# Performance work log

Hardware: AMD Instinct MI355X
Metric: run time of the kernel (lower is better)

Reference implementation:

```python
import jax, jax.numpy as jnp
import numpy as np

B, C, H, W = 4, 3, 512, 512
V, NF = 12000, 24000
UH, UW = 1024, 1024


def setup_inputs() -> dict:
    key = jax.random.key(0)
    ks = jax.random.split(key, 8)
    img = jax.random.normal(ks[0], (B, C, H, W), jnp.float32)
    mesh = jax.random.normal(ks[1], (B, V, 3), jnp.float32) * 0.3
    mesh = mesh.at[:, :, 2].add(3.0)  # keep depth positive so projection is well-defined
    face = jax.random.randint(ks[2], (NF, 3), 0, V, jnp.int32)
    focal = 800.0 + 200.0 * jax.random.uniform(ks[3], (B, 2), jnp.float32)
    princpt = jnp.tile(jnp.array([[W / 2.0, H / 2.0]], jnp.float32), (B, 1))
    R = jnp.tile(jnp.eye(3, dtype=jnp.float32)[None], (B, 1, 1))
    t = jnp.zeros((B, 3), jnp.float32)
    # pytorch3d packed convention: face id f of batch i is stored as f + NF*i, background = -1
    base = jax.random.randint(ks[4], (B, H, W), -1, NF, jnp.int32)
    offs = (NF * jnp.arange(B, dtype=jnp.int32))[:, None, None]
    pix_to_face_xy = jnp.where(base != -1, base + offs, -1)
    pix_to_face_uv = jax.random.randint(ks[5], (UH, UW), -1, NF, jnp.int32)
    bary = jax.random.uniform(ks[6], (UH, UW, 3), jnp.float32) + 1e-3
    bary_coords_uv = bary / bary.sum(-1, keepdims=True)
    return dict(img=img, mesh=mesh, face=face, focal=focal, princpt=princpt,
                R=R, t=t, pix_to_face_xy=pix_to_face_xy,
                pix_to_face_uv=pix_to_face_uv, bary_coords_uv=bary_coords_uv)


def _grid_sample(img, grid):
    # F.grid_sample: bilinear, align_corners=True, zero padding.
    # img [B,C,H,W], grid [B,Uh,Uw,2] in [-1,1] -> out [B,C,Uh,Uw]
    Bq, Cq, Hq, Wq = img.shape
    ix = (grid[..., 0] + 1.0) * 0.5 * (Wq - 1)
    iy = (grid[..., 1] + 1.0) * 0.5 * (Hq - 1)
    ix0 = jnp.floor(ix)
    iy0 = jnp.floor(iy)
    wx1 = ix - ix0
    wx0 = 1.0 - wx1
    wy1 = iy - iy0
    wy0 = 1.0 - wy1
    bidx = jnp.arange(Bq)[:, None, None]

    def tap(yf, xf, w):
        valid = (xf >= 0) & (xf <= Wq - 1) & (yf >= 0) & (yf <= Hq - 1)
        xi = jnp.clip(xf, 0, Wq - 1).astype(jnp.int32)
        yi = jnp.clip(yf, 0, Hq - 1).astype(jnp.int32)
        vals = img[bidx, :, yi, xi]  # [B,Uh,Uw,C]
        return vals * (w * valid)[..., None]

    out = (tap(iy0, ix0, wy0 * wx0) + tap(iy0, ix0 + 1.0, wy0 * wx1)
           + tap(iy0 + 1.0, ix0, wy1 * wx0) + tap(iy0 + 1.0, ix0 + 1.0, wy1 * wx1))
    return jnp.transpose(out, (0, 3, 1, 2))


def _forward(img, mesh, focal, princpt, R, t, bary_coords_uv,
             face, pix_to_face_xy, pix_to_face_uv):
    Bq, Cq, Hq, Wq = img.shape
    Fn = face.shape[0]
    Vn = mesh.shape[1]
    # camera transform + perspective projection
    mesh_cam = jnp.einsum('bij,bvj->bvi', R, mesh) + t[:, None, :]
    x = mesh_cam[..., 0] / mesh_cam[..., 2] * focal[:, None, 0] + princpt[:, None, 0]
    y = mesh_cam[..., 1] / mesh_cam[..., 2] * focal[:, None, 1] + princpt[:, None, 1]
    mesh_img = jnp.stack((x, y), 2)  # [B,V,2]
    # per-batch visible-face mask (packed ids: subtract Fn*i; torch's index -1 wraps
    # to face Fn-1 when scattering 1.0 -- replicate that exactly)
    local = jnp.where(pix_to_face_xy != -1,
                      pix_to_face_xy - Fn * jnp.arange(Bq, dtype=pix_to_face_xy.dtype)[:, None, None],
                      -1)
    local = jnp.where(local < 0, local + Fn, local)
    valid = jnp.zeros((Bq, Fn), jnp.float32).at[
        jnp.arange(Bq)[:, None], local.reshape(Bq, -1)].set(1.0)
    # invalidate invisible faces: vertex ids -> -1
    faces_b = jnp.where(valid[:, :, None] > 0, face[None].astype(jnp.int32), -1)  # [B,F,3]
    puv = jnp.where(pix_to_face_uv < 0, pix_to_face_uv + Fn, pix_to_face_uv)  # wrap like torch
    vidx = faces_b[:, puv, :]  # [B,UH,UW,3]
    invisible = (vidx[..., 0] == -1).astype(img.dtype)  # [B,UH,UW]
    vw = jnp.where(vidx < 0, vidx + Vn, vidx)  # -1 wraps to last vertex, like torch
    gathered = mesh_img[jnp.arange(Bq)[:, None, None, None], vw]  # [B,UH,UW,3,2]
    uvpos = jnp.einsum('bhwkc,hwk->bhwc', gathered, bary_coords_uv)  # barycentric blend
    grid = jnp.stack((uvpos[..., 0] / (Wq - 1) * 2.0 - 1.0,
                      uvpos[..., 1] / (Hq - 1) * 2.0 - 1.0), -1)
    uvmap = _grid_sample(img, grid)  # [B,C,UH,UW]
    uvmap = jnp.where((pix_to_face_uv == -1)[None, None], -1.0, uvmap)
    uvmap = uvmap * (1.0 - invisible)[:, None] - invisible[:, None]
    return uvmap


def reference(img, mesh, face, focal, princpt, R, t,
              pix_to_face_xy, pix_to_face_uv, bary_coords_uv):
    return _forward(img, mesh, focal, princpt, R, t, bary_coords_uv,
                    face, pix_to_face_xy, pix_to_face_uv)
```

## Files before the change

kernel.cpp:

```cpp
#include <hip/hip_runtime.h>

#define BQ 4
#define CQ 3
#define HQ 512
#define WQ 512
#define VN 12000
#define FN 24000
#define UHN 1024
#define UWN 1024
#define IMGPLANE (HQ * WQ)
#define VWORDS 768

typedef float fx4 __attribute__((ext_vector_type(4)));

#define MESHIMG_OFF 0u
#define VBITS_OFF   384000u
#define FD_OFF      396288u
#define IMGI_OFF    3468288u

__global__ void init_kernel(const float* __restrict__ mesh,
                            const float* __restrict__ focal,
                            const float* __restrict__ princpt,
                            const float* __restrict__ R,
                            const float* __restrict__ t,
                            float* __restrict__ mesh_img,
                            unsigned int* __restrict__ vbits) {
    int idx = blockIdx.x * blockDim.x + threadIdx.x;
    if (idx < BQ * VWORDS) vbits[idx] = 0u;
    if (idx >= BQ * VN) return;
    int b = idx / VN;
    const float* Rb = R + b * 9;
    const float* tb = t + b * 3;
    float mx = mesh[idx * 3 + 0];
    float my = mesh[idx * 3 + 1];
    float mz = mesh[idx * 3 + 2];
    float cx = Rb[0] * mx + Rb[1] * my + Rb[2] * mz + tb[0];
    float cy = Rb[3] * mx + Rb[4] * my + Rb[5] * mz + tb[1];
    float cz = Rb[6] * mx + Rb[7] * my + Rb[8] * mz + tb[2];
    float x = cx / cz * focal[b * 2 + 0] + princpt[b * 2 + 0];
    float y = cy / cz * focal[b * 2 + 1] + princpt[b * 2 + 1];
    mesh_img[idx * 2 + 0] = x;
    mesh_img[idx * 2 + 1] = y;
}

__global__ void interleave_kernel(const float* __restrict__ img,
                                  float4* __restrict__ img_i) {
    int i = blockIdx.x * blockDim.x + threadIdx.x;
    if (i >= (BQ * HQ * WQ) / 4) return;
    int g = i * 4;
    int b = g >> 18;
    int p = g & (IMGPLANE - 1);
    const float* ib = img + (size_t)b * CQ * IMGPLANE + p;
    float4 r0 = *(const float4*)(ib);
    float4 r1 = *(const float4*)(ib + IMGPLANE);
    float4 r2 = *(const float4*)(ib + 2 * IMGPLANE);
    img_i[g + 0] = make_float4(r0.x, r1.x, r2.x, 0.0f);
    img_i[g + 1] = make_float4(r0.y, r1.y, r2.y, 0.0f);
    img_i[g + 2] = make_float4(r0.z, r1.z, r2.z, 0.0f);
    img_i[g + 3] = make_float4(r0.w, r1.w, r2.w, 0.0f);
}

__global__ __launch_bounds__(256) void valid_kernel(const int4* __restrict__ ptf_xy4,
                                                    unsigned int* __restrict__ vbits) {
    __shared__ unsigned int lb[VWORDS];
    int tid = threadIdx.x;
    for (int i = tid; i < VWORDS; i += 256) lb[i] = 0u;
    __syncthreads();
    int b = blockIdx.x >> 6;
    int blkInB = blockIdx.x & 63;
    const int4* src = ptf_xy4 + ((size_t)b * IMGPLANE + blkInB * 4096) / 4;
#pragma unroll
    for (int k = 0; k < 4; ++k) {
        int4 p4 = src[tid + k * 256];
        int pv[4] = {p4.x, p4.y, p4.z, p4.w};
#pragma unroll
        for (int j = 0; j < 4; ++j) {
            int l = (pv[j] != -1) ? (pv[j] - FN * b) : -1;
            if (l < 0) l += FN;
            atomicOr(&lb[l >> 5], 1u << (l & 31));
        }
    }
    __syncthreads();
    for (int i = tid; i < VWORDS; i += 256) {
        unsigned int w = lb[i];
        if (w) atomicOr(&vbits[b * VWORDS + i], w);
    }
}

__global__ void fd_kernel(const int* __restrict__ face,
                          const float* __restrict__ mesh_img,
                          const unsigned int* __restrict__ vbits,
                          float4* __restrict__ fd) {
    int idx = blockIdx.x * blockDim.x + threadIdx.x;
    if (idx >= FN * BQ) return;
    int b = idx / FN;
    int f = idx - b * FN;
    int v0 = face[f * 3 + 0];
    int v1 = face[f * 3 + 1];
    int v2 = face[f * 3 + 2];
    const float* mi = mesh_img + (size_t)b * VN * 2;
    float4 a, c;
    a.x = mi[v0 * 2 + 0]; a.y = mi[v0 * 2 + 1];
    a.z = mi[v1 * 2 + 0]; a.w = mi[v1 * 2 + 1];
    c.x = mi[v2 * 2 + 0]; c.y = mi[v2 * 2 + 1];
    c.z = (float)((vbits[b * VWORDS + (f >> 5)] >> (f & 31)) & 1u);
    c.w = 0.0f;
    fd[(size_t)idx * 2 + 0] = a;
    fd[(size_t)idx * 2 + 1] = c;
}

__global__ __launch_bounds__(256) void uv_kernel(const float4* __restrict__ img_i,
                                                 const float4* __restrict__ fd,
                                                 const int* __restrict__ ptf_uv,
                                                 const float* __restrict__ bary,
                                                 float* __restrict__ out) {
    int blk = blockIdx.x;
    int r = blk & 7;
    int b = r >> 1;
    int pixBlk = ((blk >> 3) << 1) | (r & 1);
    int p0 = pixBlk * 1024 + (threadIdx.x << 2);

    const size_t PLANE = (size_t)UHN * UWN;

    int4 puv4 = *(const int4*)(ptf_uv + p0);
    float4 by0 = *(const float4*)(bary + (size_t)p0 * 3);
    float4 by1 = *(const float4*)(bary + (size_t)p0 * 3 + 4);
    float4 by2 = *(const float4*)(bary + (size_t)p0 * 3 + 8);

    int pin[4] = {puv4.x, puv4.y, puv4.z, puv4.w};
    float bw[12] = {by0.x, by0.y, by0.z, by0.w,
                    by1.x, by1.y, by1.z, by1.w,
                    by2.x, by2.y, by2.z, by2.w};

    const float4* fdb = fd + (size_t)b * FN * 2;
    float4 fa[4], fc[4];
    int pu[4];
#pragma unroll
    for (int k = 0; k < 4; ++k) {
        int p = pin[k];
        pu[k] = (p < 0) ? p + FN : p;
        fa[k] = fdb[pu[k] * 2 + 0];
        fc[k] = fdb[pu[k] * 2 + 1];
    }

    const float4* ibi = img_i + (size_t)b * IMGPLANE;
    float4 t00[4], t01[4], t10[4], t11[4];
    float g00[4], g01[4], g10[4], g11[4];
#pragma unroll
    for (int k = 0; k < 4; ++k) {
        float w0 = bw[3 * k + 0], w1 = bw[3 * k + 1], w2 = bw[3 * k + 2];
        float ux = w0 * fa[k].x + w1 * fa[k].z + w2 * fc[k].x;
        float uy = w0 * fa[k].y + w1 * fa[k].w + w2 * fc[k].y;

        float gx = ux / (float)(WQ - 1) * 2.0f - 1.0f;
        float gy = uy / (float)(HQ - 1) * 2.0f - 1.0f;
        float ix = (gx + 1.0f) * 0.5f * (float)(WQ - 1);
        float iy = (gy + 1.0f) * 0.5f * (float)(HQ - 1);

        float ix0 = floorf(ix), iy0 = floorf(iy);
        float wx1 = ix - ix0, wx0 = 1.0f - wx1;
        float wy1 = iy - iy0, wy0 = 1.0f - wy1;
        float ix1 = ix0 + 1.0f, iy1 = iy0 + 1.0f;

        bool x0ok = (ix0 >= 0.0f) && (ix0 <= (float)(WQ - 1));
        bool x1ok = (ix1 >= 0.0f) && (ix1 <= (float)(WQ - 1));
        bool y0ok = (iy0 >= 0.0f) && (iy0 <= (float)(HQ - 1));
        bool y1ok = (iy1 >= 0.0f) && (iy1 <= (float)(HQ - 1));

        g00[k] = (y0ok && x0ok) ? wy0 * wx0 : 0.0f;
        g01[k] = (y0ok && x1ok) ? wy0 * wx1 : 0.0f;
        g10[k] = (y1ok && x0ok) ? wy1 * wx0 : 0.0f;
        g11[k] = (y1ok && x1ok) ? wy1 * wx1 : 0.0f;

        int xi0 = (int)fminf(fmaxf(ix0, 0.0f), (float)(WQ - 1));
        int xi1 = (int)fminf(fmaxf(ix1, 0.0f), (float)(WQ - 1));
        int yi0 = (int)fminf(fmaxf(iy0, 0.0f), (float)(HQ - 1));
        int yi1 = (int)fminf(fmaxf(iy1, 0.0f), (float)(HQ - 1));

        t00[k] = ibi[yi0 * WQ + xi0];
        t01[k] = ibi[yi0 * WQ + xi1];
        t10[k] = ibi[yi1 * WQ + xi0];
        t11[k] = ibi[yi1 * WQ + xi1];
    }

    float o0[4], o1[4], o2[4];
#pragma unroll
    for (int k = 0; k < 4; ++k) {
        float acc0 = 0.f, acc1 = 0.f, acc2 = 0.f;
        acc0 += t00[k].x * g00[k]; acc1 += t00[k].y * g00[k]; acc2 += t00[k].z * g00[k];
        acc0 += t01[k].x * g01[k]; acc1 += t01[k].y * g01[k]; acc2 += t01[k].z * g01[k];
        acc0 += t10[k].x * g10[k]; acc1 += t10[k].y * g10[k]; acc2 += t10[k].z * g10[k];
        acc0 += t11[k].x * g11[k]; acc1 += t11[k].y * g11[k]; acc2 += t11[k].z * g11[k];
        bool ok = (pin[k] != -1) && (fc[k].z != 0.0f);
        o0[k] = ok ? acc0 : -1.0f;
        o1[k] = ok ? acc1 : -1.0f;
        o2[k] = ok ? acc2 : -1.0f;
    }

    float* ob = out + (size_t)b * CQ * PLANE + p0;
    fx4 s0 = {o0[0], o0[1], o0[2], o0[3]};
    fx4 s1 = {o1[0], o1[1], o1[2], o1[3]};
    fx4 s2 = {o2[0], o2[1], o2[2], o2[3]};
    __builtin_nontemporal_store(s0, (fx4*)(ob));
    __builtin_nontemporal_store(s1, (fx4*)(ob + PLANE));
    __builtin_nontemporal_store(s2, (fx4*)(ob + 2 * PLANE));
}

extern "C" void kernel_launch(void* const* d_in, const int* in_sizes, int n_in,
                              void* d_out, int out_size, void* d_ws, size_t ws_size,
                              hipStream_t stream) {
    const float* img     = (const float*)d_in[0];
    const float* mesh    = (const float*)d_in[1];
    const int*   face    = (const int*)d_in[2];
    const float* focal   = (const float*)d_in[3];
    const float* princpt = (const float*)d_in[4];
    const float* R       = (const float*)d_in[5];
    const float* t       = (const float*)d_in[6];
    const int*   ptf_xy  = (const int*)d_in[7];
    const int*   ptf_uv  = (const int*)d_in[8];
    const float* bary    = (const float*)d_in[9];
    float* out = (float*)d_out;

    unsigned char* ws = (unsigned char*)d_ws;
    float*         mesh_img = (float*)(ws + MESHIMG_OFF);
    unsigned int*  vbits    = (unsigned int*)(ws + VBITS_OFF);
    float4*        fd       = (float4*)(ws + FD_OFF);
    float4*        img_i    = (float4*)(ws + IMGI_OFF);

    init_kernel<<<(BQ * VN + 255) / 256, 256, 0, stream>>>(
        mesh, focal, princpt, R, t, mesh_img, vbits);

    interleave_kernel<<<(BQ * HQ * WQ / 4) / 256, 256, 0, stream>>>(img, img_i);

    valid_kernel<<<256, 256, 0, stream>>>((const int4*)ptf_xy, vbits);

    fd_kernel<<<(FN * BQ + 255) / 256, 256, 0, stream>>>(
        face, mesh_img, vbits, fd);

    uv_kernel<<<4096, 256, 0, stream>>>(img_i, fd, ptf_uv, bary, out);
}
```

Before: 188.5 us.

## Store interleaved image in fp16 and fuse prep kernels into one launch

The interleaved RGB image copy is now written as half precision (8 bytes per texel instead of 16), which halves the gather traffic in the bilinear-sample kernel and the write traffic of the interleave pass. The mesh projection and vbits clearing are merged into the interleave kernel, saving one launch. The uv kernel also switches its streaming input loads to nontemporal loads. Storing the image in fp16 loses precision in the sampled values and may exceed the accuracy tolerance.

```diff
diff --git a/kernel.cpp b/kernel.cpp
--- a/kernel.cpp
+++ b/kernel.cpp
@@ -11,53 +11,57 @@
 #define IMGPLANE (HQ * WQ)
 #define VWORDS 768
 
-typedef float fx4 __attribute__((ext_vector_type(4)));
+typedef float  fx4 __attribute__((ext_vector_type(4)));
+typedef int    ix4 __attribute__((ext_vector_type(4)));
+typedef _Float16 hx4 __attribute__((ext_vector_type(4)));
+typedef _Float16 hx8 __attribute__((ext_vector_type(8)));
 
 #define MESHIMG_OFF 0u
 #define VBITS_OFF   384000u
 #define FD_OFF      396288u
-#define IMGI_OFF    3468288u
-
-__global__ void init_kernel(const float* __restrict__ mesh,
-                            const float* __restrict__ focal,
-                            const float* __restrict__ princpt,
-                            const float* __restrict__ R,
-                            const float* __restrict__ t,
-                            float* __restrict__ mesh_img,
-                            unsigned int* __restrict__ vbits) {
-    int idx = blockIdx.x * blockDim.x + threadIdx.x;
-    if (idx < BQ * VWORDS) vbits[idx] = 0u;
-    if (idx >= BQ * VN) return;
-    int b = idx / VN;
-    const float* Rb = R + b * 9;
-    const float* tb = t + b * 3;
-    float mx = mesh[idx * 3 + 0];
-    float my = mesh[idx * 3 + 1];
-    float mz = mesh[idx * 3 + 2];
-    float cx = Rb[0] * mx + Rb[1] * my + Rb[2] * mz + tb[0];
-    float cy = Rb[3] * mx + Rb[4] * my + Rb[5] * mz + tb[1];
-    float cz = Rb[6] * mx + Rb[7] * my + Rb[8] * mz + tb[2];
-    float x = cx / cz * focal[b * 2 + 0] + princpt[b * 2 + 0];
-    float y = cy / cz * focal[b * 2 + 1] + princpt[b * 2 + 1];
-    mesh_img[idx * 2 + 0] = x;
-    mesh_img[idx * 2 + 1] = y;
-}
-
-__global__ void interleave_kernel(const float* __restrict__ img,
-                                  float4* __restrict__ img_i) {
-    int i = blockIdx.x * blockDim.x + threadIdx.x;
-    if (i >= (BQ * HQ * WQ) / 4) return;
+#define IMGH_OFF    3468288u
+
+__global__ __launch_bounds__(256) void prep_kernel(const float* __restrict__ img,
+                                                   const float* __restrict__ mesh,
+                                                   const float* __restrict__ focal,
+                                                   const float* __restrict__ princpt,
+                                                   const float* __restrict__ R,
+                                                   const float* __restrict__ t,
+                                                   float* __restrict__ mesh_img,
+                                                   unsigned int* __restrict__ vbits,
+                                                   _Float16* __restrict__ imgh) {
+    int i = blockIdx.x * 256 + threadIdx.x;
     int g = i * 4;
     int b = g >> 18;
     int p = g & (IMGPLANE - 1);
+
     const float* ib = img + (size_t)b * CQ * IMGPLANE + p;
     float4 r0 = *(const float4*)(ib);
     float4 r1 = *(const float4*)(ib + IMGPLANE);
     float4 r2 = *(const float4*)(ib + 2 * IMGPLANE);
-    img_i[g + 0] = make_float4(r0.x, r1.x, r2.x, 0.0f);
-    img_i[g + 1] = make_float4(r0.y, r1.y, r2.y, 0.0f);
-    img_i[g + 2] = make_float4(r0.z, r1.z, r2.z, 0.0f);
-    img_i[g + 3] = make_float4(r0.w, r1.w, r2.w, 0.0f);
+    hx8 s01 = {(_Float16)r0.x, (_Float16)r1.x, (_Float16)r2.x, (_Float16)0.f,
+               (_Float16)r0.y, (_Float16)r1.y, (_Float16)r2.y, (_Float16)0.f};
+    hx8 s23 = {(_Float16)r0.z, (_Float16)r1.z, (_Float16)r2.z, (_Float16)0.f,
+               (_Float16)r0.w, (_Float16)r1.w, (_Float16)r2.w, (_Float16)0.f};
+    *(hx8*)(imgh + (size_t)g * 4)       = s01;
+    *(hx8*)(imgh + (size_t)(g + 2) * 4) = s23;
+
+    if (i < BQ * VWORDS) vbits[i] = 0u;
+    if (i < BQ * VN) {
+        int bb = i / VN;
+        const float* Rb = R + bb * 9;
+        const float* tb = t + bb * 3;
+        float mx = mesh[i * 3 + 0];
+        float my = mesh[i * 3 + 1];
+        float mz = mesh[i * 3 + 2];
+        float cx = Rb[0] * mx + Rb[1] * my + Rb[2] * mz + tb[0];
+        float cy = Rb[3] * mx + Rb[4] * my + Rb[5] * mz + tb[1];
+        float cz = Rb[6] * mx + Rb[7] * my + Rb[8] * mz + tb[2];
+        float x = cx / cz * focal[bb * 2 + 0] + princpt[bb * 2 + 0];
+        float y = cy / cz * focal[bb * 2 + 1] + princpt[bb * 2 + 1];
+        mesh_img[i * 2 + 0] = x;
+        mesh_img[i * 2 + 1] = y;
+    }
 }
 
 __global__ __launch_bounds__(256) void valid_kernel(const int4* __restrict__ ptf_xy4,
@@ -109,7 +113,7 @@
     fd[(size_t)idx * 2 + 1] = c;
 }
 
-__global__ __launch_bounds__(256) void uv_kernel(const float4* __restrict__ img_i,
+__global__ __launch_bounds__(256) void uv_kernel(const _Float16* __restrict__ imgh,
                                                  const float4* __restrict__ fd,
                                                  const int* __restrict__ ptf_uv,
                                                  const float* __restrict__ bary,
@@ -122,15 +126,15 @@
 
     const size_t PLANE = (size_t)UHN * UWN;
 
-    int4 puv4 = *(const int4*)(ptf_uv + p0);
-    float4 by0 = *(const float4*)(bary + (size_t)p0 * 3);
-    float4 by1 = *(const float4*)(bary + (size_t)p0 * 3 + 4);
-    float4 by2 = *(const float4*)(bary + (size_t)p0 * 3 + 8);
-
-    int pin[4] = {puv4.x, puv4.y, puv4.z, puv4.w};
-    float bw[12] = {by0.x, by0.y, by0.z, by0.w,
-                    by1.x, by1.y, by1.z, by1.w,
-                    by2.x, by2.y, by2.z, by2.w};
+    ix4 puv4 = __builtin_nontemporal_load((const ix4*)(ptf_uv + p0));
+    fx4 by0 = __builtin_nontemporal_load((const fx4*)(bary + (size_t)p0 * 3));
+    fx4 by1 = __builtin_nontemporal_load((const fx4*)(bary + (size_t)p0 * 3 + 4));
+    fx4 by2 = __builtin_nontemporal_load((const fx4*)(bary + (size_t)p0 * 3 + 8));
+
+    int pin[4] = {puv4[0], puv4[1], puv4[2], puv4[3]};
+    float bw[12] = {by0[0], by0[1], by0[2], by0[3],
+                    by1[0], by1[1], by1[2], by1[3],
+                    by2[0], by2[1], by2[2], by2[3]};
 
     const float4* fdb = fd + (size_t)b * FN * 2;
     float4 fa[4], fc[4];
@@ -143,8 +147,8 @@
         fc[k] = fdb[pu[k] * 2 + 1];
     }
 
-    const float4* ibi = img_i + (size_t)b * IMGPLANE;
-    float4 t00[4], t01[4], t10[4], t11[4];
+    const _Float16* ihb = imgh + (size_t)b * IMGPLANE * 4;
+    hx4 t00[4], t01[4], t10[4], t11[4];
     float g00[4], g01[4], g10[4], g11[4];
 #pragma unroll
     for (int k = 0; k < 4; ++k) {
@@ -177,20 +181,20 @@
         int yi0 = (int)fminf(fmaxf(iy0, 0.0f), (float)(HQ - 1));
         int yi1 = (int)fminf(fmaxf(iy1, 0.0f), (float)(HQ - 1));
 
-        t00[k] = ibi[yi0 * WQ + xi0];
-        t01[k] = ibi[yi0 * WQ + xi1];
-        t10[k] = ibi[yi1 * WQ + xi0];
-        t11[k] = ibi[yi1 * WQ + xi1];
+        t00[k] = *(const hx4*)(ihb + (size_t)(yi0 * WQ + xi0) * 4);
+        t01[k] = *(const hx4*)(ihb + (size_t)(yi0 * WQ + xi1) * 4);
+        t10[k] = *(const hx4*)(ihb + (size_t)(yi1 * WQ + xi0) * 4);
+        t11[k] = *(const hx4*)(ihb + (size_t)(yi1 * WQ + xi1) * 4);
     }
 
     float o0[4], o1[4], o2[4];
 #pragma unroll
     for (int k = 0; k < 4; ++k) {
         float acc0 = 0.f, acc1 = 0.f, acc2 = 0.f;
-        acc0 += t00[k].x * g00[k]; acc1 += t00[k].y * g00[k]; acc2 += t00[k].z * g00[k];
-        acc0 += t01[k].x * g01[k]; acc1 += t01[k].y * g01[k]; acc2 += t01[k].z * g01[k];
-        acc0 += t10[k].x * g10[k]; acc1 += t10[k].y * g10[k]; acc2 += t10[k].z * g10[k];
-        acc0 += t11[k].x * g11[k]; acc1 += t11[k].y * g11[k]; acc2 += t11[k].z * g11[k];
+        acc0 += (float)t00[k][0] * g00[k]; acc1 += (float)t00[k][1] * g00[k]; acc2 += (float)t00[k][2] * g00[k];
+        acc0 += (float)t01[k][0] * g01[k]; acc1 += (float)t01[k][1] * g01[k]; acc2 += (float)t01[k][2] * g01[k];
+        acc0 += (float)t10[k][0] * g10[k]; acc1 += (float)t10[k][1] * g10[k]; acc2 += (float)t10[k][2] * g10[k];
+        acc0 += (float)t11[k][0] * g11[k]; acc1 += (float)t11[k][1] * g11[k]; acc2 += (float)t11[k][2] * g11[k];
         bool ok = (pin[k] != -1) && (fc[k].z != 0.0f);
         o0[k] = ok ? acc0 : -1.0f;
         o1[k] = ok ? acc1 : -1.0f;
@@ -225,17 +229,15 @@
     float*         mesh_img = (float*)(ws + MESHIMG_OFF);
     unsigned int*  vbits    = (unsigned int*)(ws + VBITS_OFF);
     float4*        fd       = (float4*)(ws + FD_OFF);
-    float4*        img_i    = (float4*)(ws + IMGI_OFF);
-
-    init_kernel<<<(BQ * VN + 255) / 256, 256, 0, stream>>>(
-        mesh, focal, princpt, R, t, mesh_img, vbits);
-
-    interleave_kernel<<<(BQ * HQ * WQ / 4) / 256, 256, 0, stream>>>(img, img_i);
+    _Float16*      imgh     = (_Float16*)(ws + IMGH_OFF);
+
+    prep_kernel<<<1024, 256, 0, stream>>>(
+        img, mesh, focal, princpt, R, t, mesh_img, vbits, imgh);
 
     valid_kernel<<<256, 256, 0, stream>>>((const int4*)ptf_xy, vbits);
 
     fd_kernel<<<(FN * BQ + 255) / 256, 256, 0, stream>>>(
         face, mesh_img, vbits, fd);
 
-    uv_kernel<<<4096, 256, 0, stream>>>(img_i, fd, ptf_uv, bary, out);
-}
+    uv_kernel<<<4096, 256, 0, stream>>>(imgh, fd, ptf_uv, bary, out);
+}
```

Measured after the change: 189.2 us. No clear change (+0.3%).
